# Kernel tuning notes

Hardware: AMD Instinct MI355X
Metric: run time of the kernel (lower is better)

The kernel has to match this reference:

```python
import jax, jax.numpy as jnp
import numpy as np

N, E, DIN, HID, H, ED = 50000, 800000, 128, 64, 4, 5
Z_IDX = 3          # impedance column
PHYS_W = 1.0       # physics_weight
NEG_SLOPE = 0.2    # GATv2 leaky_relu slope


def gat_layer(x, src, dst, ea, Wl, bl, Wr, br, We, att, temp, bias, concat):
    """PhysicsGATv2Conv (add_self_loops=False, eval mode / no dropout)."""
    n = x.shape[0]
    Hh, C = att.shape
    xl = (x @ Wl + bl).reshape(n, Hh, C)   # lin_l -> source features
    xr = (x @ Wr + br).reshape(n, Hh, C)   # lin_r -> target features
    # physics-enhanced edge attr: overwrite last column with temp * w / |Z|
    z = jnp.clip(ea[:, Z_IDX], 1e-6, None)
    ea = ea.at[:, -1].set(temp * PHYS_W / z)
    e = (ea @ We).reshape(-1, Hh, C)       # lin_edge (no bias)
    m = jax.nn.leaky_relu(xl[src] + xr[dst] + e, NEG_SLOPE)  # [E,H,C]
    logit = jnp.einsum('ehc,hc->eh', m, att)                 # [E,H]
    # segment softmax over incoming edges of each target node
    lmax = jax.ops.segment_max(logit, dst, num_segments=n)
    w = jnp.exp(logit - lmax[dst])
    den = jax.ops.segment_sum(w, dst, num_segments=n)
    a = w / (den[dst] + 1e-16)
    out = jax.ops.segment_sum(xl[src] * a[:, :, None], dst, num_segments=n)
    out = out.reshape(n, Hh * C) if concat else out.mean(axis=1)
    return out + bias


def layer_norm(x, w, b):
    mu = x.mean(-1, keepdims=True)
    v = ((x - mu) ** 2).mean(-1, keepdims=True)
    return (x - mu) * jax.lax.rsqrt(v + 1e-5) * w + b


def setup_inputs() -> dict:
    key = jax.random.key(0)
    ks = iter(jax.random.split(key, 40))
    nk = lambda: next(ks)
    d = {}
    d['x'] = jax.random.normal(nk(), (N, DIN), jnp.float32)
    d['edge_index'] = jax.random.randint(nk(), (2, E), 0, N)
    d['edge_attr'] = jax.random.uniform(nk(), (E, ED), jnp.float32)
    hd = HID * H
    cfg = [(DIN, True), (hd, True), (hd, False)]
    for i, (din, concat) in enumerate(cfg):
        dout = hd if concat else HID
        d[f'Wl{i}'] = jax.random.normal(nk(), (din, hd), jnp.float32) / np.sqrt(din)
        d[f'bl{i}'] = 0.01 * jax.random.normal(nk(), (hd,), jnp.float32)
        d[f'Wr{i}'] = jax.random.normal(nk(), (din, hd), jnp.float32) / np.sqrt(din)
        d[f'br{i}'] = 0.01 * jax.random.normal(nk(), (hd,), jnp.float32)
        d[f'We{i}'] = jax.random.normal(nk(), (ED, hd), jnp.float32) / np.sqrt(ED)
        d[f'att{i}'] = jax.random.normal(nk(), (H, HID), jnp.float32) / np.sqrt(HID)
        d[f'temp{i}'] = jnp.float32(1.0)
        d[f'bias{i}'] = 0.01 * jax.random.normal(nk(), (dout,), jnp.float32)
        d[f'lnw{i}'] = jnp.ones((dout,), jnp.float32)
        d[f'lnb{i}'] = jnp.zeros((dout,), jnp.float32)
    d['pw0'] = jax.random.normal(nk(), (DIN, hd), jnp.float32) / np.sqrt(DIN)
    d['pb0'] = jnp.zeros((hd,), jnp.float32)
    d['pw2'] = jax.random.normal(nk(), (hd, HID), jnp.float32) / np.sqrt(hd)
    d['pb2'] = jnp.zeros((HID,), jnp.float32)
    return d


def reference(x, edge_index, edge_attr,
              Wl0, bl0, Wr0, br0, We0, att0, temp0, bias0, lnw0, lnb0,
              Wl1, bl1, Wr1, br1, We1, att1, temp1, bias1, lnw1, lnb1,
              Wl2, bl2, Wr2, br2, We2, att2, temp2, bias2, lnw2, lnb2,
              pw0, pb0, pw2, pb2):
    src, dst = edge_index[0], edge_index[1]
    # layer 0: 128 -> 256 (concat), residual projected
    h = gat_layer(x, src, dst, edge_attr, Wl0, bl0, Wr0, br0, We0, att0, temp0, bias0, True)
    h = layer_norm(h, lnw0, lnb0) + (x @ pw0 + pb0)
    h = jax.nn.elu(h)
    # layer 1: 256 -> 256 (concat), identity residual
    h1 = gat_layer(h, src, dst, edge_attr, Wl1, bl1, Wr1, br1, We1, att1, temp1, bias1, True)
    h = layer_norm(h1, lnw1, lnb1) + h
    h = jax.nn.elu(h)
    # layer 2: 256 -> 64 (head-mean), residual projected, no activation
    h2 = gat_layer(h, src, dst, edge_attr, Wl2, bl2, Wr2, br2, We2, att2, temp2, bias2, False)
    out = layer_norm(h2, lnw2, lnb2) + (h @ pw2 + pb2)
    return out
```

## Files before the change

### kernel.cpp

```cpp
#include <hip/hip_runtime.h>
#include <math.h>

#define NN 50000
#define EE 800000
#define NB 196

typedef _Float16 half8 __attribute__((ext_vector_type(8)));
typedef _Float16 hv4  __attribute__((ext_vector_type(4)));
typedef float floatx16 __attribute__((ext_vector_type(16)));
typedef float fv4 __attribute__((ext_vector_type(4)));

__device__ __forceinline__ float fexp2(float x) { return __builtin_amdgcn_exp2f(x); }

template<int CTRL>
__device__ __forceinline__ float dppadd(float x) {
    int t = __builtin_amdgcn_update_dpp(0, __float_as_int(x), CTRL, 0xf, 0xf, false);
    return x + __int_as_float(t);
}
__device__ __forceinline__ float red16(float x) {
    x = dppadd<0x121>(x);
    x = dppadd<0x122>(x);
    x = dppadd<0x124>(x);
    x = dppadd<0x128>(x);
    return x;
}

__global__ __launch_bounds__(256) void swizzleA(
    const float* __restrict__ A, _Float16* __restrict__ Asw, int M, int K)
{
    int wave = threadIdx.x >> 6, lane = threadIdx.x & 63;
    int tile = blockIdx.x;
    int kc = blockIdx.y * 4 + wave;
    int KC = K >> 4;
    int row = tile * 32 + (lane & 31);
    int k0 = kc * 16 + (lane >> 5) * 8;
    float4 v0 = make_float4(0.f, 0.f, 0.f, 0.f);
    float4 v1 = make_float4(0.f, 0.f, 0.f, 0.f);
    if (row < M) {
        const float* p = A + (size_t)row * K + k0;
        v0 = *(const float4*)p;
        v1 = *(const float4*)(p + 4);
    }
    half8 o;
    o[0] = (_Float16)v0.x; o[1] = (_Float16)v0.y;
    o[2] = (_Float16)v0.z; o[3] = (_Float16)v0.w;
    o[4] = (_Float16)v1.x; o[5] = (_Float16)v1.y;
    o[6] = (_Float16)v1.z; o[7] = (_Float16)v1.w;
    *(half8*)(Asw + (((size_t)tile * KC + kc) * 64 + lane) * 8) = o;
}

__global__ __launch_bounds__(256) void prep_weights(
    const float* __restrict__ s0, const float* __restrict__ s1,
    const float* __restrict__ s2, const float* __restrict__ s3,
    const float* __restrict__ s4, const float* __restrict__ s5,
    const float* __restrict__ s6, const float* __restrict__ s7,
    _Float16* __restrict__ catB0, _Float16* __restrict__ catB1,
    _Float16* __restrict__ catB2,
    const float* __restrict__ bl0, const float* __restrict__ br0,
    const float* __restrict__ pb0, const float* __restrict__ bl1,
    const float* __restrict__ br1, const float* __restrict__ bl2,
    const float* __restrict__ br2, const float* __restrict__ pb2,
    float* __restrict__ cb0, float* __restrict__ cb1, float* __restrict__ cb2)
{
    int b = blockIdx.x;
    if (b >= 184) {
        int t = (b - 184) * 256 + threadIdx.x;
        if (t < 768) {
            cb0[t] = (t < 256) ? bl0[t] : (t < 512) ? br0[t - 256] : pb0[t - 512];
        } else if (t < 1280) {
            int u = t - 768;
            cb1[u] = (u < 256) ? bl1[u] : br1[u - 256];
        } else if (t < 1856) {
            int u = t - 1280;
            cb2[u] = (u < 256) ? bl2[u] : (u < 512) ? br2[u - 256] : pb2[u - 512];
        }
        return;
    }
    int wave = threadIdx.x >> 6, lane = threadIdx.x & 63;
    int pair = b * 4 + wave;
    const int cum[9] = {0, 64, 128, 192, 320, 448, 576, 704, 736};
    int job = 0;
    while (pair >= cum[job + 1]) ++job;
    const float* srcs[8] = {s0, s1, s2, s3, s4, s5, s6, s7};
    const int KCs[8] = {8, 8, 8, 16, 16, 16, 16, 16};
    const int NCs[8] = {256, 256, 256, 256, 256, 256, 256, 64};
    const int ntb[8] = {0, 8, 16, 0, 8, 0, 8, 16};
    _Float16* dsts[8] = {catB0, catB0, catB0, catB1, catB1, catB2, catB2, catB2};
    int p = pair - cum[job];
    int KC = KCs[job], NC = NCs[job];
    int nt = p / KC, kc = p - nt * KC;
    int n = nt * 32 + (lane & 31);
    int k0 = kc * 16 + (lane >> 5) * 8;
    const float* B = srcs[job];
    half8 o;
#pragma unroll
    for (int jj = 0; jj < 8; ++jj)
        o[jj] = (_Float16)B[(size_t)(k0 + jj) * NC + n];
    int ntG = ntb[job] + nt;
    *(half8*)(dsts[job] + (((size_t)ntG * KC + kc) * 64 + lane) * 8) = o;
}

template<int CT>
__global__ __launch_bounds__(256) void gemm_mfma(
    const _Float16* __restrict__ Asw, const _Float16* __restrict__ Bsw,
    const float* __restrict__ bias, _Float16* __restrict__ C,
    int M, int K, int NC)
{
    const int wave = threadIdx.x >> 6, lane = threadIdx.x & 63;
    const int KC = K >> 4;
    const int rt0 = blockIdx.x * 4 + (wave & 1) * 2;
    const int ct0 = blockIdx.y * (2 * CT) + (wave >> 1) * CT;

    const half8* Ap0 = (const half8*)Asw + (size_t)rt0 * KC * 64 + lane;
    const half8* Ap1 = Ap0 + (size_t)KC * 64;
    const half8* Bp0 = (const half8*)Bsw + (size_t)ct0 * KC * 64 + lane;
    const half8* Bp1 = Bp0 + (size_t)KC * 64;

    floatx16 acc00 = {0.f}, acc10 = {0.f}, acc01 = {0.f}, acc11 = {0.f};

    for (int kc = 0; kc < KC; ++kc) {
        half8 a0 = Ap0[(size_t)kc * 64];
        half8 a1 = Ap1[(size_t)kc * 64];
        half8 b0 = Bp0[(size_t)kc * 64];
        acc00 = __builtin_amdgcn_mfma_f32_32x32x16_f16(a0, b0, acc00, 0, 0, 0);
        acc10 = __builtin_amdgcn_mfma_f32_32x32x16_f16(a1, b0, acc10, 0, 0, 0);
        if (CT == 2) {
            half8 b1 = Bp1[(size_t)kc * 64];
            acc01 = __builtin_amdgcn_mfma_f32_32x32x16_f16(a0, b1, acc01, 0, 0, 0);
            acc11 = __builtin_amdgcn_mfma_f32_32x32x16_f16(a1, b1, acc11, 0, 0, 0);
        }
    }

    const int nlane = lane & 31, hs = lane >> 5;
#pragma unroll
    for (int c = 0; c < CT; ++c) {
        int col = (ct0 + c) * 32 + nlane;
        float bb = bias[col];
        const floatx16& a_ = (c == 0) ? acc00 : acc01;
        const floatx16& b_ = (c == 0) ? acc10 : acc11;
#pragma unroll
        for (int r = 0; r < 16; ++r) {
            int rowin = (r & 3) + 8 * (r >> 2) + 4 * hs;
            int row0 = rt0 * 32 + rowin;
            int row1 = row0 + 32;
            if (row0 < M) C[(size_t)row0 * NC + col] = (_Float16)(a_[r] + bb);
            if (row1 < M) C[(size_t)row1 * NC + col] = (_Float16)(b_[r] + bb);
        }
    }
}

__global__ __launch_bounds__(256) void hist_kernel(const int* __restrict__ dst,
                                                   int* __restrict__ deg)
{
    int e = blockIdx.x * 256 + threadIdx.x;
    if (e < EE) atomicAdd(&deg[dst[e]], 1);
}

__global__ __launch_bounds__(256) void scan_local(const int* __restrict__ deg,
                                                  int* __restrict__ rowoff,
                                                  int* __restrict__ part)
{
    __shared__ int sd[256];
    int tid = threadIdx.x;
    int i = blockIdx.x * 256 + tid;
    int v = (i < NN) ? deg[i] : 0;
    sd[tid] = v;
    __syncthreads();
    for (int off = 1; off < 256; off <<= 1) {
        int t = (tid >= off) ? sd[tid - off] : 0;
        __syncthreads();
        sd[tid] += t;
        __syncthreads();
    }
    if (i < NN) rowoff[i] = sd[tid] - v;
    if (tid == 255) part[blockIdx.x] = sd[255];
}

__global__ __launch_bounds__(256) void scan_part(int* __restrict__ part,
                                                 int* __restrict__ rowoff)
{
    __shared__ int sd[256];
    int tid = threadIdx.x;
    int v = (tid < NB) ? part[tid] : 0;
    sd[tid] = v;
    __syncthreads();
    for (int off = 1; off < 256; off <<= 1) {
        int t = (tid >= off) ? sd[tid - off] : 0;
        __syncthreads();
        sd[tid] += t;
        __syncthreads();
    }
    if (tid < NB) part[tid] = sd[tid] - v;
    if (tid == 0) rowoff[NN] = EE;
}

__global__ __launch_bounds__(256) void scan_add(int* __restrict__ rowoff,
                                                const int* __restrict__ part,
                                                int* __restrict__ cursor)
{
    int i = blockIdx.x * 256 + threadIdx.x;
    if (i < NN) {
        rowoff[i] += part[blockIdx.x];
        cursor[i] = 0;
    }
}

__global__ __launch_bounds__(256) void scatter_kernel(
    const int* __restrict__ src, const int* __restrict__ dst,
    const float* __restrict__ ea, const int* __restrict__ rowoff,
    int* __restrict__ cursor, int* __restrict__ srcp,
    float4* __restrict__ eap, float* __restrict__ erec)
{
    int e = blockIdx.x * 256 + threadIdx.x;
    if (e < EE) {
        int d = dst[e];
        int pos = rowoff[d] + atomicAdd(&cursor[d], 1);
        srcp[pos] = src[e];
        const float* p = ea + (size_t)e * 5;
        eap[pos] = make_float4(p[0], p[1], p[2], p[3]);
        erec[pos] = 1.0f / fmaxf(p[3], 1e-6f);
    }
}

__global__ __launch_bounds__(256) void fused_attn_ln(
    const int* __restrict__ rowoff, const int* __restrict__ srcp,
    const float4* __restrict__ eap, const float* __restrict__ erec,
    const _Float16* __restrict__ xlp, int rstride,
    const float* __restrict__ We, const float* __restrict__ att,
    const float* __restrict__ temp, const float* __restrict__ bias,
    const float* __restrict__ lnw, const float* __restrict__ lnb,
    const _Float16* __restrict__ residH, const float* __restrict__ residF,
    float* __restrict__ outF, _Float16* __restrict__ aswOut, int mode)
{
    int v = __builtin_amdgcn_readfirstlane(blockIdx.x * 4 + (threadIdx.x >> 6));
    int lane = threadIdx.x & 63;
    if (v >= NN) return;
    int grp = lane >> 4;
    int sub = lane & 15;
    int j = grp * 64 + sub * 4;

    fv4 ww0 = *(const fv4*)(We + j);
    fv4 ww1 = *(const fv4*)(We + 256 + j);
    fv4 ww2 = *(const fv4*)(We + 512 + j);
    fv4 ww3 = *(const fv4*)(We + 768 + j);
    fv4 ww4 = *(const fv4*)(We + 1024 + j);
    fv4 atv = *(const fv4*)(att + j);
    fv4 xrv = __builtin_convertvector(
        *(const hv4*)(xlp + (size_t)v * rstride + 256 + j), fv4);
    float tmp = temp[0];
    const float L2E = 1.44269504088896340736f;

    float mxd = -INFINITY, dend = 0.f;
    fv4 acc = {0.f, 0.f, 0.f, 0.f};

    int beg = rowoff[v], end = rowoff[v + 1];
    int i = beg;
    for (; i + 2 <= end; i += 2) {
        int s0 = srcp[i], s1 = srcp[i + 1];
        float4 a0 = eap[i], a1 = eap[i + 1];
        float q0 = tmp * erec[i], q1 = tmp * erec[i + 1];
        fv4 x0 = __builtin_convertvector(
            *(const hv4*)(xlp + (size_t)s0 * rstride + j), fv4);
        fv4 x1 = __builtin_convertvector(
            *(const hv4*)(xlp + (size_t)s1 * rstride + j), fv4);
        fv4 m0 = x0 + xrv;
        m0 = m0 + a0.x * ww0; m0 = m0 + a0.y * ww1; m0 = m0 + a0.z * ww2;
        m0 = m0 + a0.w * ww3; m0 = m0 + q0 * ww4;
        fv4 m1 = x1 + xrv;
        m1 = m1 + a1.x * ww0; m1 = m1 + a1.y * ww1; m1 = m1 + a1.z * ww2;
        m1 = m1 + a1.w * ww3; m1 = m1 + q1 * ww4;
        m0 = __builtin_elementwise_max(m0, m0 * 0.2f);
        m1 = __builtin_elementwise_max(m1, m1 * 0.2f);
        fv4 p0 = m0 * atv, p1 = m1 * atv;
        float l0 = (p0[0] + p0[1]) + (p0[2] + p0[3]);
        float l1 = (p1[0] + p1[1]) + (p1[2] + p1[3]);
        l0 = red16(l0) * L2E;
        l1 = red16(l1) * L2E;
        float nm = fmaxf(mxd, fmaxf(l0, l1));
        float sc = fexp2(mxd - nm);
        float e0 = fexp2(l0 - nm);
        float e1 = fexp2(l1 - nm);
        mxd = nm;
        dend = dend * sc + (e0 + e1);
        acc = acc * sc + (x0 * e0 + x1 * e1);
    }
    if (i < end) {
        int s0 = srcp[i];
        float4 a0 = eap[i];
        float q0 = tmp * erec[i];
        fv4 x0 = __builtin_convertvector(
            *(const hv4*)(xlp + (size_t)s0 * rstride + j), fv4);
        fv4 m0 = x0 + xrv;
        m0 = m0 + a0.x * ww0; m0 = m0 + a0.y * ww1; m0 = m0 + a0.z * ww2;
        m0 = m0 + a0.w * ww3; m0 = m0 + q0 * ww4;
        m0 = __builtin_elementwise_max(m0, m0 * 0.2f);
        fv4 p0 = m0 * atv;
        float l0 = (p0[0] + p0[1]) + (p0[2] + p0[3]);
        l0 = red16(l0) * L2E;
        float nm = fmaxf(mxd, l0);
        float sc = fexp2(mxd - nm);
        float e0 = fexp2(l0 - nm);
        mxd = nm;
        dend = dend * sc + e0;
        acc = acc * sc + x0 * e0;
    }

    float inv = __builtin_amdgcn_rcpf(dend + 1e-16f);
    if (mode <= 1) {
        fv4 bb = *(const fv4*)(bias + j);
        fv4 o = acc * inv + bb;
        float s  = (o[0] + o[1]) + (o[2] + o[3]);
        fv4 oq = o * o;
        float s2 = (oq[0] + oq[1]) + (oq[2] + oq[3]);
        s = red16(s);   s += __shfl_xor(s, 16, 64);  s += __shfl_xor(s, 32, 64);
        s2 = red16(s2); s2 += __shfl_xor(s2, 16, 64); s2 += __shfl_xor(s2, 32, 64);
        float mu = s * (1.f / 256.f);
        float var = s2 * (1.f / 256.f) - mu * mu;
        float rs = __builtin_amdgcn_rsqf(var + 1e-5f);
        fv4 lw = *(const fv4*)(lnw + j);
        fv4 lb = *(const fv4*)(lnb + j);
        fv4 rr;
        if (mode == 0)
            rr = __builtin_convertvector(
                *(const hv4*)(residH + (size_t)v * rstride + j), fv4);
        else
            rr = *(const fv4*)(residF + (size_t)v * 256 + j);
        fv4 y = (o - mu) * rs * lw + lb + rr;
        y[0] = (y[0] > 0.f) ? y[0] : fexp2(y[0] * L2E) - 1.f;
        y[1] = (y[1] > 0.f) ? y[1] : fexp2(y[1] * L2E) - 1.f;
        y[2] = (y[2] > 0.f) ? y[2] : fexp2(y[2] * L2E) - 1.f;
        y[3] = (y[3] > 0.f) ? y[3] : fexp2(y[3] * L2E) - 1.f;
        if (mode == 0)
            *(fv4*)(outF + (size_t)v * 256 + j) = y;
        int kc = j >> 4, half = (j >> 3) & 1, off = j & 7;
        size_t idx = (((size_t)(v >> 5) * 16 + kc) * 64 + (v & 31) + 32 * half) * 8 + off;
        hv4 yh = __builtin_convertvector(y, hv4);
        *(hv4*)(aswOut + idx) = yh;
    } else {
        fv4 r = acc * inv;
        r[0] += __shfl_xor(r[0], 16, 64); r[0] += __shfl_xor(r[0], 32, 64);
        r[1] += __shfl_xor(r[1], 16, 64); r[1] += __shfl_xor(r[1], 32, 64);
        r[2] += __shfl_xor(r[2], 16, 64); r[2] += __shfl_xor(r[2], 32, 64);
        r[3] += __shfl_xor(r[3], 16, 64); r[3] += __shfl_xor(r[3], 32, 64);
        fv4 bb = *(const fv4*)(bias + sub * 4);
        fv4 o = r * 0.25f + bb;
        float s  = (o[0] + o[1]) + (o[2] + o[3]);
        fv4 oq = o * o;
        float s2 = (oq[0] + oq[1]) + (oq[2] + oq[3]);
        s = red16(s);
        s2 = red16(s2);
        float mu = s * (1.f / 64.f);
        float var = s2 * (1.f / 64.f) - mu * mu;
        float rs = __builtin_amdgcn_rsqf(var + 1e-5f);
        fv4 lw = *(const fv4*)(lnw + sub * 4);
        fv4 lb = *(const fv4*)(lnb + sub * 4);
        fv4 rr = __builtin_convertvector(
            *(const hv4*)(residH + (size_t)v * rstride + sub * 4), fv4);
        fv4 y = (o - mu) * rs * lw + lb + rr;
        if (grp == 0)
            *(fv4*)(outF + (size_t)v * 64 + sub * 4) = y;
    }
}

extern "C" void kernel_launch(void* const* d_in, const int* in_sizes, int n_in,
                              void* d_out, int out_size, void* d_ws, size_t ws_size,
                              hipStream_t stream)
{
    const float* x    = (const float*)d_in[0];
    const int*   eidx = (const int*)d_in[1];
    const float* ea   = (const float*)d_in[2];
    const int* src = eidx;
    const int* dst = eidx + EE;

    const float *Wl[3], *bl[3], *Wr[3], *br[3], *We[3], *att[3], *temp[3],
                *bias[3], *lnw[3], *lnb[3];
    for (int i = 0; i < 3; ++i) {
        int b = 3 + i * 10;
        Wl[i]   = (const float*)d_in[b + 0];
        bl[i]   = (const float*)d_in[b + 1];
        Wr[i]   = (const float*)d_in[b + 2];
        br[i]   = (const float*)d_in[b + 3];
        We[i]   = (const float*)d_in[b + 4];
        att[i]  = (const float*)d_in[b + 5];
        temp[i] = (const float*)d_in[b + 6];
        bias[i] = (const float*)d_in[b + 7];
        lnw[i]  = (const float*)d_in[b + 8];
        lnb[i]  = (const float*)d_in[b + 9];
    }
    const float* pw0 = (const float*)d_in[33];
    const float* pb0 = (const float*)d_in[34];
    const float* pw2 = (const float*)d_in[35];
    const float* pb2 = (const float*)d_in[36];

    char* w = (char*)d_ws;
    float* h     = (float*)w; w += (size_t)NN * 256 * 4;
    char*  gbase = w;         w += (size_t)NN * 256 * 4;
    _Float16* xlr = (_Float16*)w; w += (size_t)NN * 768 * 2;
    float4* eap  = (float4*)w; w += (size_t)EE * 16;
    float* erec  = (float*)w; w += (size_t)EE * 4;
    int* srcp    = (int*)w;   w += (size_t)EE * 4;
    int* rowoff  = (int*)w;   w += (size_t)(NN + 16) * 4;
    int* cursor  = (int*)w;   w += (size_t)NN * 4;
    int* part    = (int*)w;   w += 1024;
    w = (char*)(((uintptr_t)w + 255) & ~(uintptr_t)255);
    _Float16* catB0 = (_Float16*)w; w += 196608;
    _Float16* catB1 = (_Float16*)w; w += 262144;
    _Float16* catB2 = (_Float16*)w; w += 294912;
    float* cb0 = (float*)w; w += 768 * 4;
    float* cb1 = (float*)w; w += 512 * 4;
    float* cb2 = (float*)w; w += 576 * 4;
    _Float16* Asw = (_Float16*)gbase;

    dim3 blk(256);
    dim3 grid_e((EE + 255) / 256);
    dim3 grid_nw((NN + 3) / 4);
    dim3 grid_nb(NB);
    const int MT = 391;

    auto attn = [&](int L, int rstride, const _Float16* residH,
                    const float* residF, float* outFp, _Float16* asw, int mode) {
        fused_attn_ln<<<grid_nw, blk, 0, stream>>>(
            rowoff, srcp, eap, erec, xlr, rstride, We[L], att[L], temp[L],
            bias[L], lnw[L], lnb[L], residH, residF, outFp, asw, mode);
    };

    hipMemsetAsync(cursor, 0, (size_t)NN * 4, stream);
    hipLaunchKernelGGL(hist_kernel, grid_e, blk, 0, stream, dst, cursor);
    hipLaunchKernelGGL(scan_local, grid_nb, blk, 0, stream, cursor, rowoff, part);
    hipLaunchKernelGGL(scan_part, dim3(1), blk, 0, stream, part, rowoff);
    hipLaunchKernelGGL(scan_add, grid_nb, blk, 0, stream, rowoff, part, cursor);
    hipLaunchKernelGGL(scatter_kernel, grid_e, blk, 0, stream,
                       src, dst, ea, rowoff, cursor, srcp, eap, erec);

    hipLaunchKernelGGL(prep_weights, dim3(192), blk, 0, stream,
                       Wl[0], Wr[0], pw0, Wl[1], Wr[1], Wl[2], Wr[2], pw2,
                       catB0, catB1, catB2,
                       bl[0], br[0], pb0, bl[1], br[1], bl[2], br[2], pb2,
                       cb0, cb1, cb2);

    swizzleA<<<dim3(4 * MT, 2), blk, 0, stream>>>(x, Asw, NN, 128);
    gemm_mfma<2><<<dim3(MT, 6), blk, 0, stream>>>(
        Asw, catB0, cb0, xlr, NN, 128, 768);
    attn(0, 768, xlr + 512, nullptr, h, Asw, 0);

    gemm_mfma<2><<<dim3(MT, 4), blk, 0, stream>>>(
        Asw, catB1, cb1, xlr, NN, 256, 512);
    attn(1, 512, nullptr, h, nullptr, Asw, 1);

    gemm_mfma<2><<<dim3(MT, 4), blk, 0, stream>>>(
        Asw, catB2, cb2, xlr, NN, 256, 576);
    gemm_mfma<1><<<dim3(MT, 1), blk, 0, stream>>>(
        Asw, catB2 + 131072, cb2 + 512, xlr + 512, NN, 256, 576);
    attn(2, 576, xlr + 512, nullptr, (float*)d_out, nullptr, 2);
}
```

Before: 707.4 us.

## Interleave GEMM column tiles for packed half2 stores and unroll attention by four

The weight swizzle now interleaves even and odd columns, so each GEMM wave writes adjacent column pairs as packed half2 stores instead of scattered single-half stores. This lets the layer-2 GEMM be merged into one launch, with a clamped group index covering the extra 64-column tile. The attention edge loop is unrolled from 2 to 4 edges per iteration to expose more independent gathers. The changes risk higher register pressure in the attention kernel, and clamped duplicate groups redo some work.

```diff
diff --git a/kernel.cpp b/kernel.cpp
--- a/kernel.cpp
+++ b/kernel.cpp
@@ -7,6 +7,7 @@
 
 typedef _Float16 half8 __attribute__((ext_vector_type(8)));
 typedef _Float16 hv4  __attribute__((ext_vector_type(4)));
+typedef _Float16 hv2  __attribute__((ext_vector_type(2)));
 typedef float floatx16 __attribute__((ext_vector_type(16)));
 typedef float fv4 __attribute__((ext_vector_type(4)));
 
@@ -89,7 +90,7 @@
     int p = pair - cum[job];
     int KC = KCs[job], NC = NCs[job];
     int nt = p / KC, kc = p - nt * KC;
-    int n = nt * 32 + (lane & 31);
+    int n = (nt >> 1) * 64 + ((lane & 31) * 2) + (nt & 1);
     int k0 = kc * 16 + (lane >> 5) * 8;
     const float* B = srcs[job];
     half8 o;
@@ -100,7 +101,6 @@
     *(half8*)(dsts[job] + (((size_t)ntG * KC + kc) * 64 + lane) * 8) = o;
 }
 
-template<int CT>
 __global__ __launch_bounds__(256) void gemm_mfma(
     const _Float16* __restrict__ Asw, const _Float16* __restrict__ Bsw,
     const float* __restrict__ bias, _Float16* __restrict__ C,
@@ -109,42 +109,48 @@
     const int wave = threadIdx.x >> 6, lane = threadIdx.x & 63;
     const int KC = K >> 4;
     const int rt0 = blockIdx.x * 4 + (wave & 1) * 2;
-    const int ct0 = blockIdx.y * (2 * CT) + (wave >> 1) * CT;
+    const int NG = NC >> 6;
+    int g = blockIdx.y * 2 + (wave >> 1);
+    if (g >= NG) g = NG - 1;
 
     const half8* Ap0 = (const half8*)Asw + (size_t)rt0 * KC * 64 + lane;
     const half8* Ap1 = Ap0 + (size_t)KC * 64;
-    const half8* Bp0 = (const half8*)Bsw + (size_t)ct0 * KC * 64 + lane;
+    const half8* Bp0 = (const half8*)Bsw + (size_t)(2 * g) * KC * 64 + lane;
     const half8* Bp1 = Bp0 + (size_t)KC * 64;
 
-    floatx16 acc00 = {0.f}, acc10 = {0.f}, acc01 = {0.f}, acc11 = {0.f};
-
+    floatx16 accE0 = {0.f}, accE1 = {0.f}, accO0 = {0.f}, accO1 = {0.f};
+
+#pragma unroll 4
     for (int kc = 0; kc < KC; ++kc) {
         half8 a0 = Ap0[(size_t)kc * 64];
         half8 a1 = Ap1[(size_t)kc * 64];
         half8 b0 = Bp0[(size_t)kc * 64];
-        acc00 = __builtin_amdgcn_mfma_f32_32x32x16_f16(a0, b0, acc00, 0, 0, 0);
-        acc10 = __builtin_amdgcn_mfma_f32_32x32x16_f16(a1, b0, acc10, 0, 0, 0);
-        if (CT == 2) {
-            half8 b1 = Bp1[(size_t)kc * 64];
-            acc01 = __builtin_amdgcn_mfma_f32_32x32x16_f16(a0, b1, acc01, 0, 0, 0);
-            acc11 = __builtin_amdgcn_mfma_f32_32x32x16_f16(a1, b1, acc11, 0, 0, 0);
+        half8 b1 = Bp1[(size_t)kc * 64];
+        accE0 = __builtin_amdgcn_mfma_f32_32x32x16_f16(a0, b0, accE0, 0, 0, 0);
+        accE1 = __builtin_amdgcn_mfma_f32_32x32x16_f16(a1, b0, accE1, 0, 0, 0);
+        accO0 = __builtin_amdgcn_mfma_f32_32x32x16_f16(a0, b1, accO0, 0, 0, 0);
+        accO1 = __builtin_amdgcn_mfma_f32_32x32x16_f16(a1, b1, accO1, 0, 0, 0);
+    }
+
+    const int nlane = lane & 31, hs = lane >> 5;
+    int colb = g * 64 + nlane * 2;
+    float be = bias[colb], bo = bias[colb + 1];
+#pragma unroll
+    for (int r = 0; r < 16; ++r) {
+        int rowin = (r & 3) + 8 * (r >> 2) + 4 * hs;
+        int row0 = rt0 * 32 + rowin;
+        int row1 = row0 + 32;
+        if (row0 < M) {
+            hv2 pe;
+            pe[0] = (_Float16)(accE0[r] + be);
+            pe[1] = (_Float16)(accO0[r] + bo);
+            *(hv2*)(C + (size_t)row0 * NC + colb) = pe;
         }
-    }
-
-    const int nlane = lane & 31, hs = lane >> 5;
-#pragma unroll
-    for (int c = 0; c < CT; ++c) {
-        int col = (ct0 + c) * 32 + nlane;
-        float bb = bias[col];
-        const floatx16& a_ = (c == 0) ? acc00 : acc01;
-        const floatx16& b_ = (c == 0) ? acc10 : acc11;
-#pragma unroll
-        for (int r = 0; r < 16; ++r) {
-            int rowin = (r & 3) + 8 * (r >> 2) + 4 * hs;
-            int row0 = rt0 * 32 + rowin;
-            int row1 = row0 + 32;
-            if (row0 < M) C[(size_t)row0 * NC + col] = (_Float16)(a_[r] + bb);
-            if (row1 < M) C[(size_t)row1 * NC + col] = (_Float16)(b_[r] + bb);
+        if (row1 < M) {
+            hv2 po;
+            po[0] = (_Float16)(accE1[r] + be);
+            po[1] = (_Float16)(accO1[r] + bo);
+            *(hv2*)(C + (size_t)row1 * NC + colb) = po;
         }
     }
 }
@@ -255,36 +261,42 @@
 
     int beg = rowoff[v], end = rowoff[v + 1];
     int i = beg;
-    for (; i + 2 <= end; i += 2) {
-        int s0 = srcp[i], s1 = srcp[i + 1];
-        float4 a0 = eap[i], a1 = eap[i + 1];
-        float q0 = tmp * erec[i], q1 = tmp * erec[i + 1];
-        fv4 x0 = __builtin_convertvector(
-            *(const hv4*)(xlp + (size_t)s0 * rstride + j), fv4);
-        fv4 x1 = __builtin_convertvector(
-            *(const hv4*)(xlp + (size_t)s1 * rstride + j), fv4);
-        fv4 m0 = x0 + xrv;
-        m0 = m0 + a0.x * ww0; m0 = m0 + a0.y * ww1; m0 = m0 + a0.z * ww2;
-        m0 = m0 + a0.w * ww3; m0 = m0 + q0 * ww4;
-        fv4 m1 = x1 + xrv;
-        m1 = m1 + a1.x * ww0; m1 = m1 + a1.y * ww1; m1 = m1 + a1.z * ww2;
-        m1 = m1 + a1.w * ww3; m1 = m1 + q1 * ww4;
-        m0 = __builtin_elementwise_max(m0, m0 * 0.2f);
-        m1 = __builtin_elementwise_max(m1, m1 * 0.2f);
-        fv4 p0 = m0 * atv, p1 = m1 * atv;
-        float l0 = (p0[0] + p0[1]) + (p0[2] + p0[3]);
-        float l1 = (p1[0] + p1[1]) + (p1[2] + p1[3]);
-        l0 = red16(l0) * L2E;
-        l1 = red16(l1) * L2E;
-        float nm = fmaxf(mxd, fmaxf(l0, l1));
+    for (; i + 4 <= end; i += 4) {
+        int s[4]; float4 a[4]; float q[4]; fv4 xv[4]; float l[4];
+#pragma unroll
+        for (int u = 0; u < 4; ++u) {
+            s[u] = srcp[i + u];
+            a[u] = eap[i + u];
+            q[u] = tmp * erec[i + u];
+        }
+#pragma unroll
+        for (int u = 0; u < 4; ++u)
+            xv[u] = __builtin_convertvector(
+                *(const hv4*)(xlp + (size_t)s[u] * rstride + j), fv4);
+#pragma unroll
+        for (int u = 0; u < 4; ++u) {
+            fv4 m = xv[u] + xrv;
+            m = m + a[u].x * ww0; m = m + a[u].y * ww1; m = m + a[u].z * ww2;
+            m = m + a[u].w * ww3; m = m + q[u] * ww4;
+            m = __builtin_elementwise_max(m, m * 0.2f);
+            fv4 p = m * atv;
+            l[u] = (p[0] + p[1]) + (p[2] + p[3]);
+        }
+#pragma unroll
+        for (int u = 0; u < 4; ++u) l[u] = red16(l[u]) * L2E;
+        float nm = fmaxf(fmaxf(l[0], l[1]), fmaxf(l[2], l[3]));
+        nm = fmaxf(nm, mxd);
         float sc = fexp2(mxd - nm);
-        float e0 = fexp2(l0 - nm);
-        float e1 = fexp2(l1 - nm);
+        float e0 = fexp2(l[0] - nm);
+        float e1 = fexp2(l[1] - nm);
+        float e2 = fexp2(l[2] - nm);
+        float e3 = fexp2(l[3] - nm);
         mxd = nm;
-        dend = dend * sc + (e0 + e1);
-        acc = acc * sc + (x0 * e0 + x1 * e1);
-    }
-    if (i < end) {
+        dend = dend * sc + ((e0 + e1) + (e2 + e3));
+        acc = acc * sc +
+              ((xv[0] * e0 + xv[1] * e1) + (xv[2] * e2 + xv[3] * e3));
+    }
+    for (; i < end; ++i) {
         int s0 = srcp[i];
         float4 a0 = eap[i];
         float q0 = tmp * erec[i];
@@ -439,17 +451,15 @@
                        cb0, cb1, cb2);
 
     swizzleA<<<dim3(4 * MT, 2), blk, 0, stream>>>(x, Asw, NN, 128);
-    gemm_mfma<2><<<dim3(MT, 6), blk, 0, stream>>>(
+    gemm_mfma<<<dim3(MT, 6), blk, 0, stream>>>(
         Asw, catB0, cb0, xlr, NN, 128, 768);
     attn(0, 768, xlr + 512, nullptr, h, Asw, 0);
 
-    gemm_mfma<2><<<dim3(MT, 4), blk, 0, stream>>>(
+    gemm_mfma<<<dim3(MT, 4), blk, 0, stream>>>(
         Asw, catB1, cb1, xlr, NN, 256, 512);
     attn(1, 512, nullptr, h, nullptr, Asw, 1);
 
-    gemm_mfma<2><<<dim3(MT, 4), blk, 0, stream>>>(
+    gemm_mfma<<<dim3(MT, 5), blk, 0, stream>>>(
         Asw, catB2, cb2, xlr, NN, 256, 576);
-    gemm_mfma<1><<<dim3(MT, 1), blk, 0, stream>>>(
-        Asw, catB2 + 131072, cb2 + 512, xlr + 512, NN, 256, 576);
     attn(2, 576, xlr + 512, nullptr, (float*)d_out, nullptr, 2);
 }
```

Result: faster. 656.3 us (-7.2%).
